# Optimization experiments

Hardware: AMD Instinct MI355X
Metric: run time of the kernel (lower is better)

Reference implementation:

```python
import jax, jax.numpy as jnp
import numpy as np

B, T, W, L, H = 32, 1024, 512, 12, 8
CH = W // H                      # per-head dim = 64
IN_CH = 3 + 6 + T                # x + params + class embedding channels = 1033
DFF = 4 * W
NEG = -100000.0
SCALE = 1.0 / np.sqrt(np.sqrt(CH))


def _layernorm(x, g, b, eps=1e-5):
    m = jnp.mean(x, axis=-1, keepdims=True)
    v = jnp.mean(jnp.square(x - m), axis=-1, keepdims=True)
    return (x - m) * jax.lax.rsqrt(v + eps) * g + b


def setup_inputs() -> dict:
    key = jax.random.key(0)
    ks = jax.random.split(key, 40)
    std = 0.25 * np.sqrt(1.0 / W)  # init_scale used inside Transformer

    def n(k, shape, s=std):
        return (jax.random.normal(k, shape, jnp.float32) * s).astype(jnp.float32)

    inp = {
        'x': jax.random.normal(ks[0], (B, 3, T), jnp.float32),
        'params': jax.random.normal(ks[1], (B, 6, T), jnp.float32),
        'mask': (jax.random.uniform(ks[2], (B, T)) > 0.2).astype(jnp.float32),
        'class_emb': jax.random.normal(ks[3], (T, T), jnp.float32),  # nn.Embedding(n_ctx, n_ctx)
        'w_in': n(ks[4], (IN_CH, W), 0.02), 'b_in': jnp.zeros((W,), jnp.float32),
        'ln_pre_g': jnp.ones((W,), jnp.float32), 'ln_pre_b': jnp.zeros((W,), jnp.float32),
        'qkv_w': n(ks[5], (L, W, 3 * W)), 'qkv_b': jnp.zeros((L, 3 * W), jnp.float32),
        'attn_pw': n(ks[6], (L, W, W)), 'attn_pb': jnp.zeros((L, W), jnp.float32),
        'ln1_g': jnp.ones((L, W), jnp.float32), 'ln1_b': jnp.zeros((L, W), jnp.float32),
        'fc_w': n(ks[7], (L, W, DFF)), 'fc_b': jnp.zeros((L, DFF), jnp.float32),
        'fcp_w': n(ks[8], (L, DFF, W)), 'fcp_b': jnp.zeros((L, W), jnp.float32),
        'ln2_g': jnp.ones((L, W), jnp.float32), 'ln2_b': jnp.zeros((L, W), jnp.float32),
        'ln_post_g': jnp.ones((W,), jnp.float32), 'ln_post_b': jnp.zeros((W,), jnp.float32),
        'w_out': n(ks[9], (W, W), 0.02), 'b_out': jnp.zeros((W,), jnp.float32),
        'agg_fc_w': n(ks[10], (W, DFF)), 'agg_fc_b': jnp.zeros((DFF,), jnp.float32),
        'agg_pw': n(ks[11], (DFF, W)), 'agg_pb': jnp.zeros((W,), jnp.float32),
    }
    return inp


def _block(h, p):
    qw, qb, pw, pb, l1g, l1b, fw, fb, gw, gb, l2g, l2b = p
    hn = _layernorm(h, l1g, l1b)
    qkv = (hn @ qw + qb).reshape(B, T, H, 3 * CH)
    q, k, v = jnp.split(qkv, 3, axis=-1)
    att = jnp.einsum('bthc,bshc->bhts', q * SCALE, k * SCALE)
    att = jax.nn.softmax(att.astype(jnp.float32), axis=-1)  # softmax in fp32
    o = jnp.einsum('bhts,bshc->bthc', att, v).reshape(B, T, W)
    h = h + o @ pw + pb
    hn2 = _layernorm(h, l2g, l2b)
    h = h + jax.nn.gelu(hn2 @ fw + fb, approximate=False) @ gw + gb
    return h, None


def reference(x, params, mask, class_emb, w_in, b_in, ln_pre_g, ln_pre_b,
              qkv_w, qkv_b, attn_pw, attn_pb, ln1_g, ln1_b, fc_w, fc_b,
              fcp_w, fcp_b, ln2_g, ln2_b, ln_post_g, ln_post_b, w_out, b_out,
              agg_fc_w, agg_fc_b, agg_pw, agg_pb):
    # concatenate params and class-embedding channels: [B, 1033, T]
    ce = jnp.broadcast_to(class_emb.T[None], (B, T, T))  # class_embed.transpose(1,2)
    xin = jnp.concatenate([x, params, ce], axis=1)
    h = jnp.einsum('bct,cw->btw', xin, w_in) + b_in      # input_proj on [B,T,1033]
    h = _layernorm(h, ln_pre_g, ln_pre_b)
    h, _ = jax.lax.scan(_block, h,
                        (qkv_w, qkv_b, attn_pw, attn_pb, ln1_g, ln1_b,
                         fc_w, fc_b, fcp_w, fcp_b, ln2_g, ln2_b))
    h = _layernorm(h, ln_post_g, ln_post_b)
    h = (h @ w_out + b_out).transpose(0, 2, 1)           # [B, 512, T]
    h = h * mask[:, None, :]
    pooled = jnp.max(h + (1.0 - mask[:, None, :]) * NEG, axis=2)  # [B, 512]
    z = jax.nn.gelu(pooled @ agg_fc_w + agg_fc_b, approximate=False) @ agg_pw + agg_pb
    return (z, h)
```

## Files before the change

kernel.cpp:

```cpp
#include <hip/hip_runtime.h>
#include <hip/hip_bf16.h>


typedef unsigned short u16;
typedef unsigned int u32;
typedef __attribute__((ext_vector_type(8))) short bf16x8;
typedef __attribute__((ext_vector_type(8))) unsigned short us8;
typedef __attribute__((ext_vector_type(4))) unsigned short us4;
typedef __attribute__((ext_vector_type(4))) float f32x4;

__device__ __forceinline__ float bf2f(u16 s) {
  union { u32 u; float f; } c; c.u = ((u32)s) << 16; return c.f;
}
__device__ __forceinline__ u16 f2bf(float f) {
  __hip_bfloat16 h = __float2bfloat16(f);
  union { __hip_bfloat16 h; u16 u; } c; c.h = h; return c.u;
}
__device__ __forceinline__ float gelu_f(float v) {
  return 0.5f * v * (1.0f + erff(v * 0.7071067811865475f));
}
__device__ __forceinline__ void gl2lds16(const u16* g, u16* l) {
  __builtin_amdgcn_global_load_lds((const __attribute__((address_space(1))) void*)g,
                                   (__attribute__((address_space(3))) void*)l, 16, 0, 0);
}
__device__ __forceinline__ f32x4 mfma16(bf16x8 a, bf16x8 b, f32x4 c) {
  return __builtin_amdgcn_mfma_f32_16x16x32_bf16(a, b, c, 0, 0, 0);
}
__device__ __forceinline__ int swz(int row) { return (row ^ (row >> 3)) & 7; }

template <int EPI>
__global__ __launch_bounds__(512)
void gemm_bt(const u16* __restrict__ A, const u16* __restrict__ Bt,
             const float* __restrict__ bias, float* __restrict__ Cf,
             u16* __restrict__ Cb, u16* __restrict__ Vt, int K, int lda, int ldb, int ldc)
{
  __shared__ __align__(16) u16 As[2][256 * 32];
  __shared__ __align__(16) u16 Bs[2][128 * 32];
  const int tid = threadIdx.x;
  const int lane = tid & 63, wid = tid >> 6;
  const int wm = wid & 3, wn = wid >> 2;
  const int nbx = gridDim.x;
  const int nwg = nbx * gridDim.y;
  int lin = blockIdx.y * nbx + blockIdx.x;
  lin = (lin & 7) * (nwg >> 3) + (lin >> 3);
  const long m0 = (long)(lin / nbx) * 256, n0 = (long)(lin % nbx) * 128;

  const int c0 = tid, c1 = tid + 512;
  const u16* aS0 = A + (m0 + (c0 >> 2)) * (long)lda + (c0 & 3) * 8;
  const u16* aS1 = A + (m0 + (c1 >> 2)) * (long)lda + (c1 & 3) * 8;
  const u16* bS0 = Bt + (n0 + (tid >> 2)) * (long)ldb + (tid & 3) * 8;

  f32x4 acc[4][4] = {};
  const int aro = (wm * 64 + (lane & 15)) * 32 + (lane >> 4) * 8;
  const int bro = (wn * 64 + (lane & 15)) * 32 + (lane >> 4) * 8;
  const int nt = K >> 5;

#define STAGE_AB(buf, k0_)                          \
  gl2lds16(aS0 + (k0_), As[buf] + c0 * 8);          \
  gl2lds16(aS1 + (k0_), As[buf] + c1 * 8);          \
  gl2lds16(bS0 + (k0_), Bs[buf] + tid * 8);

  STAGE_AB(0, 0);
  for (int t = 0; t < nt; ++t) {
    const int cur = t & 1;
    if (t < nt - 1) {
      STAGE_AB(cur ^ 1, (t + 1) * 32);
      asm volatile("s_waitcnt vmcnt(3)" ::: "memory");
    } else {
      asm volatile("s_waitcnt vmcnt(0)" ::: "memory");
    }
    __builtin_amdgcn_s_barrier();
    bf16x8 af[4], bfr[4];
#pragma unroll
    for (int i = 0; i < 4; ++i) af[i] = *(const bf16x8*)(As[cur] + aro + i * 16 * 32);
#pragma unroll
    for (int j = 0; j < 4; ++j) bfr[j] = *(const bf16x8*)(Bs[cur] + bro + j * 16 * 32);
    __builtin_amdgcn_s_setprio(1);
#pragma unroll
    for (int i = 0; i < 4; ++i)
#pragma unroll
      for (int j = 0; j < 4; ++j)
        acc[i][j] = mfma16(af[i], bfr[j], acc[i][j]);
    __builtin_amdgcn_s_setprio(0);
    __builtin_amdgcn_s_barrier();
  }
#undef STAGE_AB
  const int rg = (lane >> 4) * 4, cl = lane & 15;
#pragma unroll
  for (int i = 0; i < 4; ++i) {
#pragma unroll
    for (int j = 0; j < 4; ++j) {
      const long row = m0 + wm * 64 + i * 16 + rg;
      const long col = n0 + wn * 64 + j * 16 + cl;
      const float bv = bias ? bias[col] : 0.0f;
      if (EPI == 4) {
        const int hh = (int)col / 192, off = (int)col - hh * 192;
        if (off < 128) {
#pragma unroll
          for (int r = 0; r < 4; ++r)
            Cb[(row + r) * ldc + col] = f2bf(acc[i][j][r] + bv);
        } else {
          us4 pk;
#pragma unroll
          for (int r = 0; r < 4; ++r) pk[r] = f2bf(acc[i][j][r] + bv);
          const long bl = row >> 10, t0 = row & 1023;
          *(us4*)(Vt + (((bl * 8 + hh) * 64 + (off - 128)) << 10) + t0) = pk;
        }
      } else {
#pragma unroll
        for (int r = 0; r < 4; ++r) {
          float v = acc[i][j][r] + bv;
          long idx = (row + r) * ldc + col;
          if (EPI == 0) Cf[idx] = v;
          else if (EPI == 1) Cb[idx] = f2bf(v);
          else if (EPI == 2) Cf[idx] += v;
          else Cb[idx] = f2bf(gelu_f(v));
        }
      }
    }
  }
}

__global__ __launch_bounds__(512)
void attn_k(const u16* __restrict__ qkv, const u16* __restrict__ vt, u16* __restrict__ o)
{
  __shared__ __align__(16) u16 Qs[128 * 64];
  __shared__ __align__(16) u16 Ks[2][64 * 64];
  __shared__ __align__(16) u16 Vts[2][64 * 64];
  const int tid = threadIdx.x, lane = tid & 63, wid = tid >> 6;
  int lin = blockIdx.x;
  lin = (lin & 7) * 128 + (lin >> 3);
  const int qt = lin & 7, hh = (lin >> 3) & 7, b = lin >> 6;
  const long rowbase = (long)b * 1024;
  const long vbase = (((long)b * 8 + hh) * 64) * 1024;
  const int g = lane >> 4, cl = lane & 15;
  u16* Psw = Qs + wid * 1024;

#pragma unroll
  for (int it = 0; it < 2; ++it) {
    int c = tid + it * 512;
    int row = c >> 3, c8s = (c & 7) ^ swz(row);
    gl2lds16(qkv + (rowbase + qt * 128 + row) * 1536 + hh * 192 + c8s * 8, Qs + c * 8);
  }
#define STAGE_KV(buf, kt_)                                                            \
  {                                                                                   \
    int row = tid >> 3, c8s = (tid & 7) ^ swz(row);                                   \
    gl2lds16(qkv + (rowbase + (kt_) * 64 + row) * 1536 + hh * 192 + 64 + c8s * 8,     \
             Ks[buf] + tid * 8);                                                      \
    gl2lds16(vt + vbase + (long)row * 1024 + (kt_) * 64 + c8s * 8, Vts[buf] + tid * 8); \
  }
  STAGE_KV(0, 0);

  float m = -3.0e38f, l = 0.f;
  f32x4 oacc[4] = {};
  const int Rq = wid * 16 + cl, sq = swz(Rq) << 3;
  const int spw = swz(cl) << 3;
  bf16x8 aq[2];

  for (int kt = 0; kt < 16; ++kt) {
    const int cur = kt & 1;
    if (kt < 15) {
      STAGE_KV(cur ^ 1, kt + 1);
      asm volatile("s_waitcnt vmcnt(2)" ::: "memory");
    } else {
      asm volatile("s_waitcnt vmcnt(0)" ::: "memory");
    }
    __builtin_amdgcn_s_barrier();
    if (kt == 0) {
#pragma unroll
      for (int kb = 0; kb < 2; ++kb)
        aq[kb] = *(const bf16x8*)(Qs + Rq * 64 + ((kb * 32 + g * 8) ^ sq));
    }
    f32x4 s[4] = {};
    __builtin_amdgcn_s_setprio(1);
#pragma unroll
    for (int j = 0; j < 4; ++j) {
      const int Rk = j * 16 + cl, sk = swz(Rk) << 3;
#pragma unroll
      for (int kb = 0; kb < 2; ++kb) {
        bf16x8 bk = *(const bf16x8*)(Ks[cur] + Rk * 64 + ((kb * 32 + g * 8) ^ sk));
        s[j] = mfma16(bk, aq[kb], s[j]);
      }
    }
    __builtin_amdgcn_s_setprio(0);
    float mx = s[0][0];
#pragma unroll
    for (int j = 0; j < 4; ++j)
#pragma unroll
      for (int r = 0; r < 4; ++r) mx = fmaxf(mx, s[j][r]);
    mx *= 0.125f;
    mx = fmaxf(mx, __shfl_xor(mx, 16, 64));
    mx = fmaxf(mx, __shfl_xor(mx, 32, 64));
    if (!__all(mx <= m + 8.f)) {
      const float mnew = fmaxf(m, mx);
      const float al = __expf(m - mnew);
      m = mnew;
      l *= al;
      float alr[4];
#pragma unroll
      for (int r = 0; r < 4; ++r) alr[r] = __shfl(al, (lane & 48) | (g * 4 + r), 64);
#pragma unroll
      for (int cb = 0; cb < 4; ++cb) {
        f32x4 t = oacc[cb];
        t[0] *= alr[0]; t[1] *= alr[1]; t[2] *= alr[2]; t[3] *= alr[3];
        oacc[cb] = t;
      }
    }
    float p[4][4], ts = 0.f;
#pragma unroll
    for (int j = 0; j < 4; ++j)
#pragma unroll
      for (int r = 0; r < 4; ++r) {
        p[j][r] = __expf(s[j][r] * 0.125f - m);
        ts += p[j][r];
      }
    ts += __shfl_xor(ts, 16, 64);
    ts += __shfl_xor(ts, 32, 64);
    l += ts;
#pragma unroll
    for (int j = 0; j < 4; ++j) {
      us4 pk;
      pk[0] = f2bf(p[j][0]); pk[1] = f2bf(p[j][1]);
      pk[2] = f2bf(p[j][2]); pk[3] = f2bf(p[j][3]);
      *(us4*)(&Psw[cl * 64 + ((j * 16 + g * 4) ^ spw)]) = pk;
    }
    asm volatile("s_waitcnt lgkmcnt(0)" ::: "memory");
    bf16x8 pa[2];
#pragma unroll
    for (int kb = 0; kb < 2; ++kb)
      pa[kb] = *(const bf16x8*)(&Psw[cl * 64 + ((kb * 32 + g * 8) ^ spw)]);
    __builtin_amdgcn_s_setprio(1);
#pragma unroll
    for (int kb = 0; kb < 2; ++kb)
#pragma unroll
      for (int cb = 0; cb < 4; ++cb) {
        const int ch = cb * 16 + cl;
        bf16x8 vb = *(const bf16x8*)(Vts[cur] + ch * 64 + ((kb * 32 + g * 8) ^ (swz(ch) << 3)));
        oacc[cb] = mfma16(pa[kb], vb, oacc[cb]);
      }
    __builtin_amdgcn_s_setprio(0);
    __builtin_amdgcn_s_barrier();
  }
#undef STAGE_KV
  float lr[4];
#pragma unroll
  for (int r = 0; r < 4; ++r) lr[r] = __shfl(l, (lane & 48) | (g * 4 + r), 64);
#pragma unroll
  for (int cb = 0; cb < 4; ++cb)
#pragma unroll
    for (int r = 0; r < 4; ++r) {
      long row = rowbase + qt * 128 + wid * 16 + g * 4 + r;
      o[row * 512 + hh * 64 + cb * 16 + cl] = f2bf(oacc[cb][r] / lr[r]);
    }
}

template <int MODE>
__global__ __launch_bounds__(256)
void ln_k(const float* __restrict__ in_, const float* __restrict__ gg,
          const float* __restrict__ bb, void* __restrict__ out_)
{
  const long row = (long)blockIdx.x * 4 + (threadIdx.x >> 6);
  const int lane = threadIdx.x & 63;
  float x[8];
  const float* p = in_ + row * 512 + lane * 8;
  *(float4*)(x) = *(const float4*)(p);
  *(float4*)(x + 4) = *(const float4*)(p + 4);
  float s = 0.f;
#pragma unroll
  for (int j = 0; j < 8; ++j) s += x[j];
#pragma unroll
  for (int off = 1; off < 64; off <<= 1) s += __shfl_xor(s, off, 64);
  const float mean = s * (1.0f / 512.0f);
  float vs = 0.f;
#pragma unroll
  for (int j = 0; j < 8; ++j) { float d = x[j] - mean; vs += d * d; }
#pragma unroll
  for (int off = 1; off < 64; off <<= 1) vs += __shfl_xor(vs, off, 64);
  const float rstd = rsqrtf(vs * (1.0f / 512.0f) + 1e-5f);
  if (MODE == 0) {
    float y[8];
#pragma unroll
    for (int j = 0; j < 8; ++j)
      y[j] = (x[j] - mean) * rstd * gg[lane * 8 + j] + bb[lane * 8 + j];
    float* q = (float*)out_ + row * 512 + lane * 8;
    *(float4*)(q) = *(const float4*)(y);
    *(float4*)(q + 4) = *(const float4*)(y + 4);
  } else {
    us8 ov;
#pragma unroll
    for (int j = 0; j < 8; ++j)
      ov[j] = f2bf((x[j] - mean) * rstd * gg[lane * 8 + j] + bb[lane * 8 + j]);
    *(us8*)((u16*)out_ + row * 512 + lane * 8) = ov;
  }
}

__global__ __launch_bounds__(256)
void embed_k(const float* __restrict__ x, const float* __restrict__ par,
             const float* __restrict__ E, const float* __restrict__ w_in,
             const float* __restrict__ b_in, float* __restrict__ h)
{
  const long bt = blockIdx.x;
  const int b = (int)(bt >> 10), t = (int)(bt & 1023);
  float xs[9];
#pragma unroll
  for (int c = 0; c < 3; ++c) xs[c] = x[((long)b * 3 + c) * 1024 + t];
#pragma unroll
  for (int c = 0; c < 6; ++c) xs[3 + c] = par[((long)b * 6 + c) * 1024 + t];
  for (int w = threadIdx.x; w < 512; w += 256) {
    float a = E[(long)t * 512 + w] + b_in[w];
#pragma unroll
    for (int c = 0; c < 9; ++c) a += xs[c] * w_in[c * 512 + w];
    h[bt * 512 + w] = a;
  }
}

__global__ __launch_bounds__(256)
void tr_k(const float* __restrict__ in, u16* __restrict__ out, int R, int C)
{
  __shared__ u16 tile[32][33];
  const int r0 = blockIdx.y * 32, c0 = blockIdx.x * 32;
  const int tx = threadIdx.x & 31, ty = threadIdx.x >> 5;
  for (int rr = ty; rr < 32; rr += 8) tile[rr][tx] = f2bf(in[(long)(r0 + rr) * C + c0 + tx]);
  __syncthreads();
  for (int rr = ty; rr < 32; rr += 8) out[(long)(c0 + rr) * R + r0 + tx] = tile[tx][rr];
}

__global__ __launch_bounds__(256)
void cast_k(const float* __restrict__ in, u16* __restrict__ out, long n)
{
  long i = ((long)blockIdx.x * 256 + threadIdx.x) * 4;
  if (i + 3 < n) {
    float4 v = *(const float4*)(in + i);
    out[i] = f2bf(v.x); out[i + 1] = f2bf(v.y); out[i + 2] = f2bf(v.z); out[i + 3] = f2bf(v.w);
  }
}

__global__ __launch_bounds__(256)
void pool1_k(const float* __restrict__ hm, const float* __restrict__ mask, float* __restrict__ part)
{
  const int c = blockIdx.x, b = blockIdx.y;
  const int t0 = c * 128;
  const int w0 = threadIdx.x, w1 = threadIdx.x + 256;
  float m0 = -3.0e38f, m1 = -3.0e38f;
  for (int t = 0; t < 128; ++t) {
    const float mv = mask[b * 1024 + t0 + t];
    const float neg = (1.0f - mv) * (-100000.0f);
    const float* row = hm + ((long)b * 1024 + t0 + t) * 512;
    m0 = fmaxf(m0, row[w0] * mv + neg);
    m1 = fmaxf(m1, row[w1] * mv + neg);
  }
  part[((long)b * 8 + c) * 512 + w0] = m0;
  part[((long)b * 8 + c) * 512 + w1] = m1;
}
__global__ __launch_bounds__(256)
void pool2_k(const float* __restrict__ part, float* __restrict__ pooled)
{
  const int b = blockIdx.y;
  const int w = blockIdx.x * 256 + threadIdx.x;
  float m = -3.0e38f;
#pragma unroll
  for (int c = 0; c < 8; ++c) m = fmaxf(m, part[((long)b * 8 + c) * 512 + w]);
  pooled[b * 512 + w] = m;
}

__global__ __launch_bounds__(256)
void tout_k(const float* __restrict__ hm, const float* __restrict__ mask, float* __restrict__ outh)
{
  __shared__ float tile[64][65];
  const int t0 = blockIdx.x * 64, w0 = blockIdx.y * 64, b = blockIdx.z;
  const int tx = threadIdx.x & 63, ty = threadIdx.x >> 6;
  for (int i = ty; i < 64; i += 4)
    tile[i][tx] = hm[((long)b * 1024 + t0 + i) * 512 + w0 + tx];
  __syncthreads();
  const float mv = mask[b * 1024 + t0 + tx];
  for (int i = ty; i < 64; i += 4)
    outh[((long)b * 512 + w0 + i) * 1024 + t0 + tx] = tile[tx][i] * mv;
}

__global__ __launch_bounds__(256)
void agg1_k(const float* __restrict__ pooled, const float* __restrict__ wf,
            const float* __restrict__ bf_, float* __restrict__ z1)
{
  const int b = blockIdx.y;
  const int n = blockIdx.x * 256 + threadIdx.x;
  float acc = 0.f;
  for (int k = 0; k < 512; ++k) acc += pooled[b * 512 + k] * wf[(long)k * 2048 + n];
  z1[(long)b * 2048 + n] = gelu_f(acc + bf_[n]);
}
__global__ __launch_bounds__(256)
void agg2_k(const float* __restrict__ z1, const float* __restrict__ wp,
            const float* __restrict__ bp, float* __restrict__ zo)
{
  const int b = blockIdx.y;
  const int n = blockIdx.x * 256 + threadIdx.x;
  float acc = 0.f;
  for (int k = 0; k < 2048; ++k) acc += z1[(long)b * 2048 + k] * wp[(long)k * 512 + n];
  zo[b * 512 + n] = acc + bp[n];
}

extern "C" void kernel_launch(void* const* d_in, const int* in_sizes, int n_in,
                              void* d_out, int out_size, void* d_ws, size_t ws_size,
                              hipStream_t stream)
{
  (void)in_sizes; (void)n_in; (void)out_size; (void)ws_size;
  const float* x        = (const float*)d_in[0];
  const float* params   = (const float*)d_in[1];
  const float* mask     = (const float*)d_in[2];
  const float* class_emb= (const float*)d_in[3];
  const float* w_in     = (const float*)d_in[4];
  const float* b_in     = (const float*)d_in[5];
  const float* ln_pre_g = (const float*)d_in[6];
  const float* ln_pre_b = (const float*)d_in[7];
  const float* qkv_w    = (const float*)d_in[8];
  const float* qkv_b    = (const float*)d_in[9];
  const float* attn_pw  = (const float*)d_in[10];
  const float* attn_pb  = (const float*)d_in[11];
  const float* ln1_g    = (const float*)d_in[12];
  const float* ln1_b    = (const float*)d_in[13];
  const float* fc_w     = (const float*)d_in[14];
  const float* fc_b     = (const float*)d_in[15];
  const float* fcp_w    = (const float*)d_in[16];
  const float* fcp_b    = (const float*)d_in[17];
  const float* ln2_g    = (const float*)d_in[18];
  const float* ln2_b    = (const float*)d_in[19];
  const float* ln_post_g= (const float*)d_in[20];
  const float* ln_post_b= (const float*)d_in[21];
  const float* w_out    = (const float*)d_in[22];
  const float* b_out    = (const float*)d_in[23];
  const float* agg_fc_w = (const float*)d_in[24];
  const float* agg_fc_b = (const float*)d_in[25];
  const float* agg_pw   = (const float*)d_in[26];
  const float* agg_pb   = (const float*)d_in[27];

  float* out_f = (float*)d_out;
  float* out_h = out_f + 16384;
  u16* sc = (u16*)out_h;

  char* ws = (char*)d_ws;
  float* hf = (float*)ws;       ws += (size_t)32768 * 512 * 4;
  u16* hn = (u16*)ws;           ws += (size_t)32768 * 512 * 2;
  float* E = (float*)ws;        ws += (size_t)1024 * 512 * 4;
  u16* ce_b = (u16*)ws;         ws += (size_t)1024 * 1024 * 2;
  u16* wt_qkv = (u16*)ws;       ws += (size_t)1536 * 512 * 2;
  u16* wt_pw  = (u16*)ws;       ws += (size_t)512 * 512 * 2;
  u16* wt_fc  = (u16*)ws;       ws += (size_t)2048 * 512 * 2;
  u16* wt_fcp = (u16*)ws;       ws += (size_t)512 * 2048 * 2;
  u16* w_in_t = (u16*)ws;       ws += (size_t)512 * 1024 * 2;
  u16* w_out_t= (u16*)ws;       ws += (size_t)512 * 512 * 2;
  float* pooled = (float*)ws;   ws += (size_t)32 * 512 * 4;
  float* z1     = (float*)ws;   ws += (size_t)32 * 2048 * 4;
  float* part   = (float*)ws;   ws += (size_t)32 * 8 * 512 * 4;
  u16* vt       = (u16*)ws;     ws += (size_t)16 * 8 * 64 * 1024 * 2;

  cast_k<<<1024, 256, 0, stream>>>(class_emb, ce_b, 1024 * 1024);
  tr_k<<<dim3(16, 32), 256, 0, stream>>>(w_in + 9 * 512, w_in_t, 1024, 512);
  tr_k<<<dim3(16, 16), 256, 0, stream>>>(w_out, w_out_t, 512, 512);
  gemm_bt<0><<<dim3(4, 4), 512, 0, stream>>>(ce_b, w_in_t, nullptr, E, nullptr, nullptr,
                                             1024, 1024, 1024, 512);
  embed_k<<<32768, 256, 0, stream>>>(x, params, E, w_in, b_in, hf);
  ln_k<0><<<8192, 256, 0, stream>>>(hf, ln_pre_g, ln_pre_b, hf);

  for (int l = 0; l < 12; ++l) {
    tr_k<<<dim3(48, 16), 256, 0, stream>>>(qkv_w + (size_t)l * 512 * 1536, wt_qkv, 512, 1536);
    tr_k<<<dim3(16, 16), 256, 0, stream>>>(attn_pw + (size_t)l * 512 * 512, wt_pw, 512, 512);
    tr_k<<<dim3(64, 16), 256, 0, stream>>>(fc_w + (size_t)l * 512 * 2048, wt_fc, 512, 2048);
    tr_k<<<dim3(16, 64), 256, 0, stream>>>(fcp_w + (size_t)l * 2048 * 512, wt_fcp, 2048, 512);

    ln_k<1><<<8192, 256, 0, stream>>>(hf, ln1_g + l * 512, ln1_b + l * 512, hn);
    for (int half = 0; half < 2; ++half) {
      const size_t ro = (size_t)half * 16384;
      gemm_bt<4><<<dim3(12, 64), 512, 0, stream>>>(hn + ro * 512, wt_qkv, qkv_b + l * 1536,
                                                   nullptr, sc, vt, 512, 512, 512, 1536);
      attn_k<<<1024, 512, 0, stream>>>(sc, vt, hn + ro * 512);
    }
    gemm_bt<2><<<dim3(4, 128), 512, 0, stream>>>(hn, wt_pw, attn_pb + l * 512,
                                                 hf, nullptr, nullptr, 512, 512, 512, 512);
    ln_k<1><<<8192, 256, 0, stream>>>(hf, ln2_g + l * 512, ln2_b + l * 512, hn);
    for (int half = 0; half < 2; ++half) {
      const size_t ro = (size_t)half * 16384;
      gemm_bt<3><<<dim3(16, 64), 512, 0, stream>>>(hn + ro * 512, wt_fc, fc_b + l * 2048,
                                                   nullptr, sc, nullptr, 512, 512, 512, 2048);
      gemm_bt<2><<<dim3(4, 64), 512, 0, stream>>>(sc, wt_fcp, fcp_b + l * 512,
                                                  hf + ro * 512, nullptr, nullptr, 2048, 2048, 2048, 512);
    }
  }

  ln_k<1><<<8192, 256, 0, stream>>>(hf, ln_post_g, ln_post_b, hn);
  gemm_bt<0><<<dim3(4, 128), 512, 0, stream>>>(hn, w_out_t, b_out, hf, nullptr, nullptr,
                                               512, 512, 512, 512);
  pool1_k<<<dim3(8, 32), 256, 0, stream>>>(hf, mask, part);
  pool2_k<<<dim3(2, 32), 256, 0, stream>>>(part, pooled);
  agg1_k<<<dim3(8, 32), 256, 0, stream>>>(pooled, agg_fc_w, agg_fc_b, z1);
  agg2_k<<<dim3(2, 32), 256, 0, stream>>>(z1, agg_pw, agg_pb, out_f);
  tout_k<<<dim3(16, 8, 32), 256, 0, stream>>>(hf, mask, out_h);
}
```

Baseline: 6.724 ms.

## Swizzle GEMM LDS tiles and split-K the aggregation MLP kernels

The GEMM now XOR-swizzles the 16-byte k-chunks of each tile row when copying from global memory into LDS, and reads them back with the matching XOR. This is meant to cut LDS bank conflicts on the fragment loads that feed the MFMA instructions. Separately, the two small aggregation matvec kernels become split-K partial kernels plus reduction kernels, which exposes more parallelism than the old 8x32 and 2x32 grids. The cost is two extra launches and some workspace for the partial sums.

```diff
diff --git a/kernel.cpp b/kernel.cpp
--- a/kernel.cpp
+++ b/kernel.cpp
@@ -46,13 +46,18 @@
   const long m0 = (long)(lin / nbx) * 256, n0 = (long)(lin % nbx) * 128;
 
   const int c0 = tid, c1 = tid + 512;
-  const u16* aS0 = A + (m0 + (c0 >> 2)) * (long)lda + (c0 & 3) * 8;
-  const u16* aS1 = A + (m0 + (c1 >> 2)) * (long)lda + (c1 & 3) * 8;
-  const u16* bS0 = Bt + (n0 + (tid >> 2)) * (long)ldb + (tid & 3) * 8;
+  const int kc0 = (c0 & 3) ^ (((c0 >> 2) >> 1) & 3);
+  const int kc1 = (c1 & 3) ^ (((c1 >> 2) >> 1) & 3);
+  const int kcb = (tid & 3) ^ (((tid >> 2) >> 1) & 3);
+  const u16* aS0 = A + (m0 + (c0 >> 2)) * (long)lda + kc0 * 8;
+  const u16* aS1 = A + (m0 + (c1 >> 2)) * (long)lda + kc1 * 8;
+  const u16* bS0 = Bt + (n0 + (tid >> 2)) * (long)ldb + kcb * 8;
 
   f32x4 acc[4][4] = {};
-  const int aro = (wm * 64 + (lane & 15)) * 32 + (lane >> 4) * 8;
-  const int bro = (wn * 64 + (lane & 15)) * 32 + (lane >> 4) * 8;
+  const int cl4 = lane & 15;
+  const int gph = ((lane >> 4) ^ ((cl4 >> 1) & 3)) * 8;
+  const int aro = (wm * 64 + cl4) * 32 + gph;
+  const int bro = (wn * 64 + cl4) * 32 + gph;
   const int nt = K >> 5;
 
 #define STAGE_AB(buf, k0_)                          \
@@ -378,23 +383,49 @@
 }
 
 __global__ __launch_bounds__(256)
-void agg1_k(const float* __restrict__ pooled, const float* __restrict__ wf,
-            const float* __restrict__ bf_, float* __restrict__ z1)
+void agg1p_k(const float* __restrict__ pooled, const float* __restrict__ wf,
+             float* __restrict__ part)
+{
+  const int b = blockIdx.z, kc = blockIdx.y;
+  const int n = blockIdx.x * 256 + threadIdx.x;
+  float acc = 0.f;
+  const int k0 = kc * 64;
+#pragma unroll 8
+  for (int k = 0; k < 64; ++k) acc += pooled[b * 512 + k0 + k] * wf[(long)(k0 + k) * 2048 + n];
+  part[((long)b * 8 + kc) * 2048 + n] = acc;
+}
+__global__ __launch_bounds__(256)
+void agg1c_k(const float* __restrict__ part, const float* __restrict__ bf_,
+             float* __restrict__ z1)
 {
   const int b = blockIdx.y;
   const int n = blockIdx.x * 256 + threadIdx.x;
   float acc = 0.f;
-  for (int k = 0; k < 512; ++k) acc += pooled[b * 512 + k] * wf[(long)k * 2048 + n];
+#pragma unroll
+  for (int c = 0; c < 8; ++c) acc += part[((long)b * 8 + c) * 2048 + n];
   z1[(long)b * 2048 + n] = gelu_f(acc + bf_[n]);
 }
 __global__ __launch_bounds__(256)
-void agg2_k(const float* __restrict__ z1, const float* __restrict__ wp,
-            const float* __restrict__ bp, float* __restrict__ zo)
+void agg2p_k(const float* __restrict__ z1, const float* __restrict__ wp,
+             float* __restrict__ part)
+{
+  const int b = blockIdx.z, kc = blockIdx.y;
+  const int n = blockIdx.x * 256 + threadIdx.x;
+  float acc = 0.f;
+  const int k0 = kc * 256;
+#pragma unroll 8
+  for (int k = 0; k < 256; ++k) acc += z1[(long)b * 2048 + k0 + k] * wp[(long)(k0 + k) * 512 + n];
+  part[((long)b * 8 + kc) * 512 + n] = acc;
+}
+__global__ __launch_bounds__(256)
+void agg2c_k(const float* __restrict__ part, const float* __restrict__ bp,
+             float* __restrict__ zo)
 {
   const int b = blockIdx.y;
   const int n = blockIdx.x * 256 + threadIdx.x;
   float acc = 0.f;
-  for (int k = 0; k < 2048; ++k) acc += z1[(long)b * 2048 + k] * wp[(long)k * 512 + n];
+#pragma unroll
+  for (int c = 0; c < 8; ++c) acc += part[((long)b * 8 + c) * 512 + n];
   zo[b * 512 + n] = acc + bp[n];
 }
 
@@ -450,6 +481,8 @@
   float* pooled = (float*)ws;   ws += (size_t)32 * 512 * 4;
   float* z1     = (float*)ws;   ws += (size_t)32 * 2048 * 4;
   float* part   = (float*)ws;   ws += (size_t)32 * 8 * 512 * 4;
+  float* apart1 = (float*)ws;   ws += (size_t)32 * 8 * 2048 * 4;
+  float* apart2 = (float*)ws;   ws += (size_t)32 * 8 * 512 * 4;
   u16* vt       = (u16*)ws;     ws += (size_t)16 * 8 * 64 * 1024 * 2;
 
   cast_k<<<1024, 256, 0, stream>>>(class_emb, ce_b, 1024 * 1024);
@@ -490,7 +523,9 @@
                                                512, 512, 512, 512);
   pool1_k<<<dim3(8, 32), 256, 0, stream>>>(hf, mask, part);
   pool2_k<<<dim3(2, 32), 256, 0, stream>>>(part, pooled);
-  agg1_k<<<dim3(8, 32), 256, 0, stream>>>(pooled, agg_fc_w, agg_fc_b, z1);
-  agg2_k<<<dim3(2, 32), 256, 0, stream>>>(z1, agg_pw, agg_pb, out_f);
+  agg1p_k<<<dim3(8, 8, 32), 256, 0, stream>>>(pooled, agg_fc_w, apart1);
+  agg1c_k<<<dim3(8, 32), 256, 0, stream>>>(apart1, agg_fc_b, z1);
+  agg2p_k<<<dim3(2, 8, 32), 256, 0, stream>>>(z1, agg_pw, apart2);
+  agg2c_k<<<dim3(2, 32), 256, 0, stream>>>(apart2, agg_pb, out_f);
   tout_k<<<dim3(16, 8, 32), 256, 0, stream>>>(hf, mask, out_h);
 }
```

After: 6.590 ms. 1.02x faster.
